# Performance work log

Measured on AMD Instinct MI355X. Metric: run time of the kernel, lower is better.

## Reference

```python
import jax, jax.numpy as jnp
import numpy as np

# Criterion config (matches init_kwargs): normalized_l2=True, count_loss_weight=1.0,
# min_count_loss_weight=1.0, zero_shot=False, aux=False -> weights {dmap:1, count:1, min_count:1}
W_DMAP, W_COUNT, W_MIN = 1.0, 1.0, 1.0


def setup_inputs() -> dict:
    key = jax.random.key(0)
    k1, k2, k3 = jax.random.split(key, 3)
    B, H, W = 32, 512, 512
    output = jax.random.uniform(k1, (B, 1, H, W), dtype=jnp.float32)
    density_map = jax.random.uniform(k2, (B, 1, H, W), dtype=jnp.float32)
    bboxes = jax.random.randint(k3, (B, 3, 4), 0, 512).astype(jnp.int64)
    return {"output": output, "density_map": density_map, "bboxes": bboxes,
            "num_objects": 96}


def _min_count_loss(output, bboxes):
    # Vectorized replacement for the per-box Python loop: one 2D integral image
    # per batch element, then 4 corner gathers per box.
    B, _, H, W = output.shape
    bb = jnp.clip(bboxes, 0, W).astype(jnp.int32)  # matches .long().clip(0, size(-1))
    o = output[:, 0]  # [B,H,W]
    # integral image with zero pad so S[y,x] = sum of o[:y,:x]
    S = jnp.pad(jnp.cumsum(jnp.cumsum(o, axis=1), axis=2), ((0, 0), (1, 0), (1, 0)))
    x1, y1, x2, y2 = bb[..., 0], bb[..., 1], bb[..., 2], bb[..., 3]
    # torch slice y1:y2 with y2<y1 is empty (sum=0); emulate via clamping
    x2 = jnp.maximum(x2, x1)
    y2 = jnp.maximum(y2, y1)
    b = jnp.arange(B)[:, None]  # [B,1] broadcast over boxes
    box_sums = S[b, y2, x2] - S[b, y1, x2] - S[b, y2, x1] + S[b, y1, x1]  # [B,nboxes]
    return jax.nn.relu(1.0 - box_sums).sum()


def reference(output, density_map, bboxes, num_objects):
    B = output.shape[0]
    # ObjectNormalizedL2Loss
    dmap_loss = jnp.sum((output - density_map) ** 2) / num_objects
    # CountLoss: MSE (mean) between per-image total counts
    diff = output.reshape(B, -1).sum(axis=1) - density_map.reshape(B, -1).sum(axis=1)
    count_loss = jnp.mean(diff ** 2)
    # MinCountLoss
    min_count = _min_count_loss(output, bboxes)
    return jnp.stack([W_DMAP * dmap_loss, W_COUNT * count_loss, W_MIN * min_count])
```

## Files before the change

kernel.cpp:

```cpp
#include <hip/hip_runtime.h>

#define BATCH 32
#define HW 262144
#define HW4 65536
#define BLOCKS_PER_BATCH 32
#define F4_PER_BLOCK 2048
#define W_IMG 512
#define N_REDUCE_BLOCKS 1024
#define N_BOX 96
#define CHUNKS_PER_BOX 16
#define N_BOX_BLOCKS 1536

#define WS_SO   0
#define WS_SD   1024
#define WS_SQ   2048
#define WS_BOX  3072

__device__ __forceinline__ double wave_reduce_d(double v) {
    for (int off = 32; off > 0; off >>= 1)
        v += __shfl_down(v, off, 64);
    return v;
}

__global__ __launch_bounds__(256) void fused_partials(const float4* __restrict__ o4,
                                                      const float4* __restrict__ d4,
                                                      const float* __restrict__ out_f,
                                                      const int* __restrict__ bb,
                                                      double* __restrict__ ws) {
    const int lane = threadIdx.x & 63;
    const int wid = threadIdx.x >> 6;
    __shared__ double sm0[4], sm1[4], sm2[4];

    if (blockIdx.x < N_REDUCE_BLOCKS) {
        const int blk = blockIdx.x;
        const size_t base = (size_t)blk * F4_PER_BLOCK;

        double so = 0.0, sd = 0.0, ssq = 0.0;
#pragma unroll
        for (int i = 0; i < 8; ++i) {
            size_t idx = base + threadIdx.x + i * 256;
            float4 a = o4[idx];
            float4 b = d4[idx];
            so += (double)a.x + (double)a.y + (double)a.z + (double)a.w;
            sd += (double)b.x + (double)b.y + (double)b.z + (double)b.w;
            double dx = (double)a.x - (double)b.x;
            double dy = (double)a.y - (double)b.y;
            double dz = (double)a.z - (double)b.z;
            double dw = (double)a.w - (double)b.w;
            ssq += dx * dx + dy * dy + dz * dz + dw * dw;
        }

        so = wave_reduce_d(so);
        sd = wave_reduce_d(sd);
        ssq = wave_reduce_d(ssq);
        if (lane == 0) { sm0[wid] = so; sm1[wid] = sd; sm2[wid] = ssq; }
        __syncthreads();
        if (threadIdx.x == 0) {
            ws[WS_SO + blk] = sm0[0] + sm0[1] + sm0[2] + sm0[3];
            ws[WS_SD + blk] = sm1[0] + sm1[1] + sm1[2] + sm1[3];
            ws[WS_SQ + blk] = sm2[0] + sm2[1] + sm2[2] + sm2[3];
        }
    } else {
        const int idx = blockIdx.x - N_REDUCE_BLOCKS;
        const int box = idx >> 4;
        const int chunk = idx & 15;
        const int b = box / 3;
        const int* p = bb + box * 4;
        int x1 = min(max(p[0], 0), W_IMG);
        int y1 = min(max(p[1], 0), W_IMG);
        int x2 = min(max(p[2], 0), W_IMG);
        int y2 = min(max(p[3], 0), W_IMG);
        x2 = max(x2, x1);
        y2 = max(y2, y1);

        const float* base = out_f + (size_t)b * HW;
        double s = 0.0;
        for (int y = y1 + chunk; y < y2; y += CHUNKS_PER_BOX) {
            const float* row = base + (size_t)y * W_IMG;
            for (int x = x1 + threadIdx.x; x < x2; x += 256)
                s += (double)row[x];
        }

        s = wave_reduce_d(s);
        if (lane == 0) sm0[wid] = s;
        __syncthreads();
        if (threadIdx.x == 0)
            ws[WS_BOX + idx] = sm0[0] + sm0[1] + sm0[2] + sm0[3];
    }
}

__global__ __launch_bounds__(1024) void finalize(const double* __restrict__ ws,
                                                 const int* __restrict__ nobj,
                                                 float* __restrict__ out) {
    const int t = threadIdx.x;
    const int lane = t & 63;
    const int wid = t >> 6;

    __shared__ double s_diff[32];
    __shared__ double s_q[16];
    __shared__ double s_m[16];

    {
        double so = ws[WS_SO + t];
        double sd = ws[WS_SD + t];
        for (int off = 16; off > 0; off >>= 1) {
            so += __shfl_down(so, off, 32);
            sd += __shfl_down(sd, off, 32);
        }
        if ((t & 31) == 0) {
            double d = so - sd;
            s_diff[t >> 5] = d * d;
        }
    }

    {
        double q = wave_reduce_d(ws[WS_SQ + t]);
        if (lane == 0) s_q[wid] = q;
    }

    {
        double m = 0.0;
        if (t < N_BOX_BLOCKS) {
            double bs = ws[WS_BOX + t];
            for (int off = 8; off > 0; off >>= 1)
                bs += __shfl_down(bs, off, 16);
            if ((t & 15) == 0) {
                m = 1.0 - bs;
                if (m < 0.0) m = 0.0;
            }
        }
        m = wave_reduce_d(m);
        if (lane == 0) s_m[wid] = m;
    }

    __syncthreads();
    if (t == 0) {
        double cnt = 0.0;
        for (int i = 0; i < 32; ++i) cnt += s_diff[i];
        double q = 0.0, m = 0.0;
        for (int i = 0; i < 16; ++i) { q += s_q[i]; m += s_m[i]; }
        out[0] = (float)(q / (double)(*nobj));
        out[1] = (float)(cnt / (double)BATCH);
        out[2] = (float)m;
    }
}

extern "C" void kernel_launch(void* const* d_in, const int* in_sizes, int n_in,
                              void* d_out, int out_size, void* d_ws, size_t ws_size,
                              hipStream_t stream) {
    const float* output  = (const float*)d_in[0];
    const float* density = (const float*)d_in[1];
    const int*   bboxes  = (const int*)d_in[2];
    const int*   numobj  = (const int*)d_in[3];
    float* out = (float*)d_out;
    double* ws = (double*)d_ws;

    fused_partials<<<N_REDUCE_BLOCKS + N_BOX_BLOCKS, 256, 0, stream>>>(
        (const float4*)output, (const float4*)density, output, bboxes, ws);

    finalize<<<1, 1024, 0, stream>>>(ws, numobj, out);
}
```

Before: 114.3 us.

## Fuse box sums into streaming reduction pass using column and row masks

Removes the 1536 separate box-sum blocks that re-read the output tensor. Each reduction block now also accumulates the three per-batch box sums over its 16-row band, using precomputed column masks and a row check on the float4 values it already loaded. The finalize kernel regroups the per-band box partials into 32 bands per box. Box sums now accumulate in float per thread rather than double, which may change rounding slightly.

```diff
diff --git a/kernel.cpp b/kernel.cpp
--- a/kernel.cpp
+++ b/kernel.cpp
@@ -3,13 +3,9 @@
 #define BATCH 32
 #define HW 262144
 #define HW4 65536
-#define BLOCKS_PER_BATCH 32
-#define F4_PER_BLOCK 2048
 #define W_IMG 512
-#define N_REDUCE_BLOCKS 1024
+#define N_BLOCKS 1024
 #define N_BOX 96
-#define CHUNKS_PER_BOX 16
-#define N_BOX_BLOCKS 1536
 
 #define WS_SO   0
 #define WS_SD   1024
@@ -24,68 +20,89 @@
 
 __global__ __launch_bounds__(256) void fused_partials(const float4* __restrict__ o4,
                                                       const float4* __restrict__ d4,
-                                                      const float* __restrict__ out_f,
                                                       const int* __restrict__ bb,
                                                       double* __restrict__ ws) {
-    const int lane = threadIdx.x & 63;
-    const int wid = threadIdx.x >> 6;
-    __shared__ double sm0[4], sm1[4], sm2[4];
+    const int blk = blockIdx.x;
+    const int batch = blk >> 5;
+    const int band = blk & 31;
+    const size_t base = (size_t)blk * 2048;
+    const int t = threadIdx.x;
+    const int col0 = (t & 127) * 4;
+    const int rbase = band * 16 + (t >> 7);
 
-    if (blockIdx.x < N_REDUCE_BLOCKS) {
-        const int blk = blockIdx.x;
-        const size_t base = (size_t)blk * F4_PER_BLOCK;
-
-        double so = 0.0, sd = 0.0, ssq = 0.0;
+    float wm[3][4];
+    int by1[3], by2[3];
+    bool active[3];
 #pragma unroll
-        for (int i = 0; i < 8; ++i) {
-            size_t idx = base + threadIdx.x + i * 256;
-            float4 a = o4[idx];
-            float4 b = d4[idx];
-            so += (double)a.x + (double)a.y + (double)a.z + (double)a.w;
-            sd += (double)b.x + (double)b.y + (double)b.z + (double)b.w;
-            double dx = (double)a.x - (double)b.x;
-            double dy = (double)a.y - (double)b.y;
-            double dz = (double)a.z - (double)b.z;
-            double dw = (double)a.w - (double)b.w;
-            ssq += dx * dx + dy * dy + dz * dz + dw * dw;
-        }
-
-        so = wave_reduce_d(so);
-        sd = wave_reduce_d(sd);
-        ssq = wave_reduce_d(ssq);
-        if (lane == 0) { sm0[wid] = so; sm1[wid] = sd; sm2[wid] = ssq; }
-        __syncthreads();
-        if (threadIdx.x == 0) {
-            ws[WS_SO + blk] = sm0[0] + sm0[1] + sm0[2] + sm0[3];
-            ws[WS_SD + blk] = sm1[0] + sm1[1] + sm1[2] + sm1[3];
-            ws[WS_SQ + blk] = sm2[0] + sm2[1] + sm2[2] + sm2[3];
-        }
-    } else {
-        const int idx = blockIdx.x - N_REDUCE_BLOCKS;
-        const int box = idx >> 4;
-        const int chunk = idx & 15;
-        const int b = box / 3;
-        const int* p = bb + box * 4;
+    for (int k = 0; k < 3; ++k) {
+        const int* p = bb + (batch * 3 + k) * 4;
         int x1 = min(max(p[0], 0), W_IMG);
         int y1 = min(max(p[1], 0), W_IMG);
         int x2 = min(max(p[2], 0), W_IMG);
         int y2 = min(max(p[3], 0), W_IMG);
         x2 = max(x2, x1);
         y2 = max(y2, y1);
+        by1[k] = y1; by2[k] = y2;
+#pragma unroll
+        for (int j = 0; j < 4; ++j) {
+            int c = col0 + j;
+            wm[k][j] = (c >= x1 && c < x2) ? 1.0f : 0.0f;
+        }
+        active[k] = (y2 > band * 16) && (y1 < band * 16 + 16);
+    }
 
-        const float* base = out_f + (size_t)b * HW;
-        double s = 0.0;
-        for (int y = y1 + chunk; y < y2; y += CHUNKS_PER_BOX) {
-            const float* row = base + (size_t)y * W_IMG;
-            for (int x = x1 + threadIdx.x; x < x2; x += 256)
-                s += (double)row[x];
+    double so = 0.0, sd = 0.0, ssq = 0.0;
+    float bxs[3] = {0.0f, 0.0f, 0.0f};
+
+#pragma unroll
+    for (int i = 0; i < 8; ++i) {
+        size_t idx = base + t + i * 256;
+        float4 a = o4[idx];
+        float4 b = d4[idx];
+        so += (double)a.x + (double)a.y + (double)a.z + (double)a.w;
+        sd += (double)b.x + (double)b.y + (double)b.z + (double)b.w;
+        double dx = (double)a.x - (double)b.x;
+        double dy = (double)a.y - (double)b.y;
+        double dz = (double)a.z - (double)b.z;
+        double dw = (double)a.w - (double)b.w;
+        ssq += dx * dx + dy * dy + dz * dz + dw * dw;
+
+        const int row = rbase + 2 * i;
+#pragma unroll
+        for (int k = 0; k < 3; ++k) {
+            if (active[k]) {
+                float rok = (row >= by1[k] && row < by2[k]) ? 1.0f : 0.0f;
+                float s = a.x * wm[k][0] + a.y * wm[k][1] + a.z * wm[k][2] + a.w * wm[k][3];
+                bxs[k] = fmaf(rok, s, bxs[k]);
+            }
         }
+    }
 
-        s = wave_reduce_d(s);
-        if (lane == 0) sm0[wid] = s;
-        __syncthreads();
-        if (threadIdx.x == 0)
-            ws[WS_BOX + idx] = sm0[0] + sm0[1] + sm0[2] + sm0[3];
+    const int lane = t & 63;
+    const int wid = t >> 6;
+    double b0 = (double)bxs[0], b1 = (double)bxs[1], b2 = (double)bxs[2];
+    so = wave_reduce_d(so);
+    sd = wave_reduce_d(sd);
+    ssq = wave_reduce_d(ssq);
+    b0 = wave_reduce_d(b0);
+    b1 = wave_reduce_d(b1);
+    b2 = wave_reduce_d(b2);
+
+    __shared__ double sm[6][4];
+    if (lane == 0) {
+        sm[0][wid] = so; sm[1][wid] = sd; sm[2][wid] = ssq;
+        sm[3][wid] = b0; sm[4][wid] = b1; sm[5][wid] = b2;
+    }
+    __syncthreads();
+    if (t == 0) {
+        ws[WS_SO + blk] = sm[0][0] + sm[0][1] + sm[0][2] + sm[0][3];
+        ws[WS_SD + blk] = sm[1][0] + sm[1][1] + sm[1][2] + sm[1][3];
+        ws[WS_SQ + blk] = sm[2][0] + sm[2][1] + sm[2][2] + sm[2][3];
+#pragma unroll
+        for (int k = 0; k < 3; ++k) {
+            double bv = sm[3 + k][0] + sm[3 + k][1] + sm[3 + k][2] + sm[3 + k][3];
+            ws[WS_BOX + (batch * 3 + k) * 32 + band] = bv;
+        }
     }
 }
 
@@ -120,13 +137,14 @@
 
     {
         double m = 0.0;
-        if (t < N_BOX_BLOCKS) {
-            double bs = ws[WS_BOX + t];
-            for (int off = 8; off > 0; off >>= 1)
-                bs += __shfl_down(bs, off, 16);
-            if ((t & 15) == 0) {
-                m = 1.0 - bs;
-                if (m < 0.0) m = 0.0;
+#pragma unroll
+        for (int k = 0; k < 3; ++k) {
+            double bs = ws[WS_BOX + t + k * 1024];
+            for (int off = 16; off > 0; off >>= 1)
+                bs += __shfl_down(bs, off, 32);
+            if ((t & 31) == 0) {
+                double r = 1.0 - bs;
+                if (r > 0.0) m += r;
             }
         }
         m = wave_reduce_d(m);
@@ -155,8 +173,8 @@
     float* out = (float*)d_out;
     double* ws = (double*)d_ws;
 
-    fused_partials<<<N_REDUCE_BLOCKS + N_BOX_BLOCKS, 256, 0, stream>>>(
-        (const float4*)output, (const float4*)density, output, bboxes, ws);
+    fused_partials<<<N_BLOCKS, 256, 0, stream>>>(
+        (const float4*)output, (const float4*)density, bboxes, ws);
 
     finalize<<<1, 1024, 0, stream>>>(ws, numobj, out);
 }
```

Measured after the change: 102.2 us. 10.6% less time.
